# Optimization experiments

Measured on AMD Instinct MI355X. Metric: run time of the kernel, lower is better.

## Reference

```python
import jax, jax.numpy as jnp
import numpy as np

B, N, H, O = 2, 512, 128, 32  # batch, n_particles, hidden_dim, obs_dim


def _linear_init(key, out_d, in_d):
    kw, kb = jax.random.split(key)
    s = 1.0 / np.sqrt(in_d)
    W = jax.random.uniform(kw, (out_d, in_d), minval=-s, maxval=s, dtype=jnp.float32)
    b = jax.random.uniform(kb, (out_d,), minval=-s, maxval=s, dtype=jnp.float32)
    return W, b


def setup_inputs() -> dict:
    key = jax.random.key(0)
    ks = jax.random.split(key, 8)
    z = jax.random.normal(ks[0], (B, N, H), dtype=jnp.float32)
    s_t = jax.random.normal(ks[1], (B, N, O), dtype=jnp.float32)
    W1, b1 = _linear_init(ks[2], H, 2 * H)   # relation_mlp layer 0
    W2, b2 = _linear_init(ks[3], H, H)       # relation_mlp layer 2
    Wq, bq = _linear_init(ks[4], H, H)       # query_proj
    Wk, bk = _linear_init(ks[5], H, O)       # key_proj
    W3, b3 = _linear_init(ks[6], H, H)       # aggregation_mlp layer 0
    W4, b4 = _linear_init(ks[7], H, H)       # aggregation_mlp layer 2
    return dict(z=z, s_t=s_t, W1=W1, b1=b1, W2=W2, b2=b2, Wq=Wq, bq=bq,
                Wk=Wk, bk=bk, W3=W3, b3=b3, W4=W4, b4=b4)


def reference(z, s_t, W1, b1, W2, b2, Wq, bq, Wk, bk, W3, b3, W4, b4):
    b_, n, h = z.shape
    # query depends only on i, key only on j (repeat in the original is redundant)
    q = z @ Wq.T + bq            # [B,N,H]
    k = s_t @ Wk.T + bk          # [B,N,H]
    scores = jnp.einsum('bih,bjh->bij', q, k) / (h ** 0.5)   # [B,N,N]
    eye = jnp.eye(n, dtype=bool)
    scores = jnp.where(eye, -jnp.inf, scores)
    attn = jax.nn.softmax(scores, axis=-1)                   # [B,N,N]
    # relation_mlp on concat(z_i, z_j): split first weight into i- and j- halves
    W1i, W1j = W1[:, :h], W1[:, h:]
    zi = z @ W1i.T               # [B,N,H]
    zj = z @ W1j.T               # [B,N,H]
    rel = jnp.tanh(zi[:, :, None, :] + zj[:, None, :, :] + b1) @ W2.T + b2  # [B,N,N,H]
    agg = jnp.einsum('bij,bijh->bih', attn, rel)             # weighted sum over j
    dz_dt = jnp.tanh(agg @ W3.T + b3) @ W4.T + b4
    return dz_dt
```

## Files before the change

### kernel.cpp

```cpp
#include <hip/hip_runtime.h>
#include <hip/hip_bf16.h>

#define NN 512
#define HH 128
#define OO 32

#define KL 2.8853900817779268f

__device__ __forceinline__ float vexp2(float x) {
    float r; asm("v_exp_f32 %0, %1" : "=v"(r) : "v"(x)); return r;
}
__device__ __forceinline__ float vrcp(float x) {
    float r; asm("v_rcp_f32 %0, %1" : "=v"(r) : "v"(x)); return r;
}
__device__ __forceinline__ float tanh_fast(float x) {
    float e = vexp2(KL * x);
    return 1.0f - 2.0f * vrcp(e + 1.0f);
}
__device__ __forceinline__ float red8(float v) {
    v += __shfl_xor(v, 1, 64); v += __shfl_xor(v, 2, 64); v += __shfl_xor(v, 4, 64);
    return v;
}
__device__ __forceinline__ float dot16r(const float4* w, const float* x, int rot) {
    float a = 0;
#pragma unroll
    for (int ii = 0; ii < 4; ii++) {
        int i = (ii + rot) & 3;
        float4 xv = *(const float4*)(x + i * 4);
        a = fmaf(xv.x, w[ii].x, a); a = fmaf(xv.y, w[ii].y, a);
        a = fmaf(xv.z, w[ii].z, a); a = fmaf(xv.w, w[ii].w, a);
    }
    return a;
}
__device__ __forceinline__ unsigned short f2bf(float x) {
    unsigned u = __float_as_uint(x);
    u += 0x7fffu + ((u >> 16) & 1u);
    return (unsigned short)(u >> 16);
}
__device__ __forceinline__ float bf_lo(unsigned u) { return __uint_as_float((u & 0xffffu) << 16); }
__device__ __forceinline__ float bf_hi(unsigned u) { return __uint_as_float(u & 0xffff0000u); }

__global__ __launch_bounds__(1024, 4) void prep_kernel(
    const float* __restrict__ z, const float* __restrict__ s_t,
    const float* __restrict__ W1, const float* __restrict__ b1,
    const float* __restrict__ Wq, const float* __restrict__ bq,
    const float* __restrict__ Wk, const float* __restrict__ bk,
    float* __restrict__ qP, float* __restrict__ cP,
    unsigned short* __restrict__ EzjG, unsigned* __restrict__ kTp) {
    __shared__ float zrow[4][HH];
    __shared__ float srow[4][OO];
    int t = threadIdx.x, bid = blockIdx.x;
    int r0 = bid * 4, b = bid >> 7, i0 = (bid & 127) * 4;
    int kq = t & 7, h = t >> 3, rot = (kq >> 1) & 3;

    const float4* WqP = (const float4*)(Wq + (size_t)h * HH) + kq * 4;
    const float4* WiP = (const float4*)(W1 + (size_t)h * 2 * HH) + kq * 4;
    const float4* WjP = (const float4*)(W1 + (size_t)h * 2 * HH + HH) + kq * 4;
    float4 wq[4], wi[4], wj[4];
#pragma unroll
    for (int ii = 0; ii < 4; ii++) {
        wq[ii] = WqP[(ii + rot) & 3];
        wi[ii] = WiP[(ii + rot) & 3];
        wj[ii] = WjP[(ii + rot) & 3];
    }
    float4 wk = ((const float4*)(Wk + (size_t)h * OO))[kq];
    float vbq = bq[h], vb1 = b1[h], vbk = bk[h];

    if (t < 4 * HH) zrow[t >> 7][t & 127] = z[(size_t)r0 * HH + t];
    else if (t < 4 * HH + 4 * OO) {
        int u = t - 4 * HH;
        srow[u >> 5][u & 31] = s_t[(size_t)r0 * OO + u];
    }
    __syncthreads();

    {
        float a0 = red8(dot16r(wq, &zrow[0][kq * 16], rot));
        float a1 = red8(dot16r(wq, &zrow[1][kq * 16], rot));
        float a2 = red8(dot16r(wq, &zrow[2][kq * 16], rot));
        float a3 = red8(dot16r(wq, &zrow[3][kq * 16], rot));
        if (kq == 0) {
            float* qp = qP + (size_t)bid * 512 + h * 4;
            qp[0] = a0 + vbq; qp[1] = a1 + vbq; qp[2] = a2 + vbq; qp[3] = a3 + vbq;
        }
    }
    {
        float a0 = red8(dot16r(wi, &zrow[0][kq * 16], rot));
        float a1 = red8(dot16r(wi, &zrow[1][kq * 16], rot));
        float a2 = red8(dot16r(wi, &zrow[2][kq * 16], rot));
        float a3 = red8(dot16r(wi, &zrow[3][kq * 16], rot));
        if (kq == 0) {
            float* cp = cP + (size_t)bid * 512 + h * 4;
            cp[0] = vexp2(KL * (a0 + vb1)); cp[1] = vexp2(KL * (a1 + vb1));
            cp[2] = vexp2(KL * (a2 + vb1)); cp[3] = vexp2(KL * (a3 + vb1));
        }
    }
    {
        float a0 = red8(dot16r(wj, &zrow[0][kq * 16], rot));
        float a1 = red8(dot16r(wj, &zrow[1][kq * 16], rot));
        float a2 = red8(dot16r(wj, &zrow[2][kq * 16], rot));
        float a3 = red8(dot16r(wj, &zrow[3][kq * 16], rot));
        if (kq == 0) {
            EzjG[(size_t)(r0 + 0) * HH + h] = f2bf(vexp2(KL * a0));
            EzjG[(size_t)(r0 + 1) * HH + h] = f2bf(vexp2(KL * a1));
            EzjG[(size_t)(r0 + 2) * HH + h] = f2bf(vexp2(KL * a2));
            EzjG[(size_t)(r0 + 3) * HH + h] = f2bf(vexp2(KL * a3));
        }
    }
    {
        float4 s0 = *(const float4*)&srow[0][kq * 4];
        float4 s1 = *(const float4*)&srow[1][kq * 4];
        float4 s2 = *(const float4*)&srow[2][kq * 4];
        float4 s3 = *(const float4*)&srow[3][kq * 4];
        float a0 = red8(s0.x * wk.x + s0.y * wk.y + s0.z * wk.z + s0.w * wk.w);
        float a1 = red8(s1.x * wk.x + s1.y * wk.y + s1.z * wk.z + s1.w * wk.w);
        float a2 = red8(s2.x * wk.x + s2.y * wk.y + s2.z * wk.z + s2.w * wk.w);
        float a3 = red8(s3.x * wk.x + s3.y * wk.y + s3.z * wk.z + s3.w * wk.w);
        if (kq == 0) {
            unsigned p01 = (unsigned)f2bf(a0 + vbk) | ((unsigned)f2bf(a1 + vbk) << 16);
            unsigned p23 = (unsigned)f2bf(a2 + vbk) | ((unsigned)f2bf(a3 + vbk) << 16);
            unsigned* kp = kTp + ((size_t)b * HH + h) * 256 + (i0 >> 1);
            kp[0] = p01; kp[1] = p23;
        }
    }
}

__global__ __launch_bounds__(1024, 4) void fused_kernel(
    const float* __restrict__ qP, const float* __restrict__ cP,
    const unsigned* __restrict__ kTp, const unsigned short* __restrict__ EzjG,
    const float* __restrict__ W2, const float* __restrict__ b2,
    const float* __restrict__ W3, const float* __restrict__ b3,
    const float* __restrict__ W4, const float* __restrict__ b4,
    float* __restrict__ out) {
    __shared__ float q4T[HH][4];
    __shared__ float c4T[HH][4];
    __shared__ float eBuf[16][4][32];
    __shared__ float sliceS[16][4];
    __shared__ float part[16][4][HH];
    __shared__ float UL[4][HH];
    __shared__ float aggL[4][HH];
    __shared__ float h1L[4][HH];

    int t = threadIdx.x, bid = blockIdx.x;
    int b = bid >> 7, i0 = (bid & 127) * 4, r0 = bid * 4;
    int w = t >> 6, lane = t & 63;

    if (t < 512) ((float*)q4T)[t] = qP[(size_t)bid * 512 + t];
    else         ((float*)c4T)[t - 512] = cP[(size_t)bid * 512 + (t - 512)];
    __syncthreads();

    {
        int jp_local = lane & 15, hq = lane >> 4;
        int jp = w * 16 + jp_local, h0 = hq * 32;
        const unsigned* kb = kTp + ((size_t)b * HH + h0) * 256 + jp;
        float s0l = 0, s1l = 0, s2l = 0, s3l = 0;
        float s0h = 0, s1h = 0, s2h = 0, s3h = 0;
#pragma unroll 8
        for (int hh = 0; hh < 32; hh++) {
            unsigned u = kb[(size_t)hh * 256];
            float kl = bf_lo(u), kh = bf_hi(u);
            float4 qv = *(const float4*)q4T[h0 + hh];
            s0l = fmaf(qv.x, kl, s0l); s1l = fmaf(qv.y, kl, s1l);
            s2l = fmaf(qv.z, kl, s2l); s3l = fmaf(qv.w, kl, s3l);
            s0h = fmaf(qv.x, kh, s0h); s1h = fmaf(qv.y, kh, s1h);
            s2h = fmaf(qv.z, kh, s2h); s3h = fmaf(qv.w, kh, s3h);
        }
        s0l += __shfl_xor(s0l, 16, 64); s0l += __shfl_xor(s0l, 32, 64);
        s1l += __shfl_xor(s1l, 16, 64); s1l += __shfl_xor(s1l, 32, 64);
        s2l += __shfl_xor(s2l, 16, 64); s2l += __shfl_xor(s2l, 32, 64);
        s3l += __shfl_xor(s3l, 16, 64); s3l += __shfl_xor(s3l, 32, 64);
        s0h += __shfl_xor(s0h, 16, 64); s0h += __shfl_xor(s0h, 32, 64);
        s1h += __shfl_xor(s1h, 16, 64); s1h += __shfl_xor(s1h, 32, 64);
        s2h += __shfl_xor(s2h, 16, 64); s2h += __shfl_xor(s2h, 32, 64);
        s3h += __shfl_xor(s3h, 16, 64); s3h += __shfl_xor(s3h, 32, 64);

        const float sc = 0.08838834764831845f;
        float e0l = __expf(s0l * sc), e1l = __expf(s1l * sc);
        float e2l = __expf(s2l * sc), e3l = __expf(s3l * sc);
        float e0h = __expf(s0h * sc), e1h = __expf(s1h * sc);
        float e2h = __expf(s2h * sc), e3h = __expf(s3h * sc);
        int jl = jp * 2, jh = jl + 1;
        if (jl == i0 + 0) e0l = 0.0f;  if (jh == i0 + 0) e0h = 0.0f;
        if (jl == i0 + 1) e1l = 0.0f;  if (jh == i0 + 1) e1h = 0.0f;
        if (jl == i0 + 2) e2l = 0.0f;  if (jh == i0 + 2) e2h = 0.0f;
        if (jl == i0 + 3) e3l = 0.0f;  if (jh == i0 + 3) e3h = 0.0f;

        float ts0 = e0l + e0h, ts1 = e1l + e1h, ts2 = e2l + e2h, ts3 = e3l + e3h;
#pragma unroll
        for (int m = 1; m <= 8; m <<= 1) {
            ts0 += __shfl_xor(ts0, m, 64); ts1 += __shfl_xor(ts1, m, 64);
            ts2 += __shfl_xor(ts2, m, 64); ts3 += __shfl_xor(ts3, m, 64);
        }
        if (lane == 0) {
            sliceS[w][0] = ts0; sliceS[w][1] = ts1;
            sliceS[w][2] = ts2; sliceS[w][3] = ts3;
        }
        if (hq == 0) {
            *(float2*)&eBuf[w][0][2 * jp_local] = make_float2(e0l, e0h);
            *(float2*)&eBuf[w][1][2 * jp_local] = make_float2(e1l, e1h);
            *(float2*)&eBuf[w][2][2 * jp_local] = make_float2(e2l, e2h);
            *(float2*)&eBuf[w][3][2 * jp_local] = make_float2(e3l, e3h);
        }

        int hp = lane * 2, jb = w * 32;
        const unsigned* zbU = (const unsigned*)EzjG + (size_t)b * NN * 64 + lane;
        float4 cA = *(const float4*)c4T[hp];
        float4 cB = *(const float4*)c4T[hp + 1];
        float a0A = 0, a1A = 0, a2A = 0, a3A = 0;
        float a0B = 0, a1B = 0, a2B = 0, a3B = 0;
#pragma unroll 8
        for (int jj = 0; jj < 32; jj++) {
            unsigned u = zbU[(size_t)(jb + jj) * 64];
            float Ex = bf_lo(u), Ey = bf_hi(u);
            float w0 = eBuf[w][0][jj], w1 = eBuf[w][1][jj];
            float w2 = eBuf[w][2][jj], w3 = eBuf[w][3][jj];
            a0A = fmaf(w0, vrcp(fmaf(cA.x, Ex, 1.0f)), a0A);
            a1A = fmaf(w1, vrcp(fmaf(cA.y, Ex, 1.0f)), a1A);
            a2A = fmaf(w2, vrcp(fmaf(cA.z, Ex, 1.0f)), a2A);
            a3A = fmaf(w3, vrcp(fmaf(cA.w, Ex, 1.0f)), a3A);
            a0B = fmaf(w0, vrcp(fmaf(cB.x, Ey, 1.0f)), a0B);
            a1B = fmaf(w1, vrcp(fmaf(cB.y, Ey, 1.0f)), a1B);
            a2B = fmaf(w2, vrcp(fmaf(cB.z, Ey, 1.0f)), a2B);
            a3B = fmaf(w3, vrcp(fmaf(cB.w, Ey, 1.0f)), a3B);
        }
        *(float2*)&part[w][0][hp] = make_float2(a0A, a0B);
        *(float2*)&part[w][1][hp] = make_float2(a1A, a1B);
        *(float2*)&part[w][2][hp] = make_float2(a2A, a2B);
        *(float2*)&part[w][3][hp] = make_float2(a3A, a3B);
    }
    __syncthreads();

    if (t < 512) {
        int r = t >> 7, h = t & 127;
        float s = 0, S = 0;
#pragma unroll
        for (int q = 0; q < 16; q++) { s += part[q][r][h]; S += sliceS[q][r]; }
        UL[r][h] = fmaf(-2.0f * vrcp(S), s, 1.0f);
    }
    __syncthreads();

    {
        int kq = t & 7, h8 = t >> 3, rot = (kq >> 1) & 3;
        float4 wv[4];
        {
            const float4* Wp = (const float4*)(W2 + (size_t)h8 * HH) + kq * 4;
#pragma unroll
            for (int ii = 0; ii < 4; ii++) wv[ii] = Wp[(ii + rot) & 3];
            float a0 = red8(dot16r(wv, &UL[0][kq * 16], rot));
            float a1 = red8(dot16r(wv, &UL[1][kq * 16], rot));
            float a2 = red8(dot16r(wv, &UL[2][kq * 16], rot));
            float a3 = red8(dot16r(wv, &UL[3][kq * 16], rot));
            if (kq == 0) {
                float vb = b2[h8];
                aggL[0][h8] = a0 + vb; aggL[1][h8] = a1 + vb;
                aggL[2][h8] = a2 + vb; aggL[3][h8] = a3 + vb;
            }
        }
        __syncthreads();
        {
            const float4* Wp = (const float4*)(W3 + (size_t)h8 * HH) + kq * 4;
#pragma unroll
            for (int ii = 0; ii < 4; ii++) wv[ii] = Wp[(ii + rot) & 3];
            float a0 = red8(dot16r(wv, &aggL[0][kq * 16], rot));
            float a1 = red8(dot16r(wv, &aggL[1][kq * 16], rot));
            float a2 = red8(dot16r(wv, &aggL[2][kq * 16], rot));
            float a3 = red8(dot16r(wv, &aggL[3][kq * 16], rot));
            if (kq == 0) {
                float vb = b3[h8];
                h1L[0][h8] = tanh_fast(a0 + vb); h1L[1][h8] = tanh_fast(a1 + vb);
                h1L[2][h8] = tanh_fast(a2 + vb); h1L[3][h8] = tanh_fast(a3 + vb);
            }
        }
        __syncthreads();
        {
            const float4* Wp = (const float4*)(W4 + (size_t)h8 * HH) + kq * 4;
#pragma unroll
            for (int ii = 0; ii < 4; ii++) wv[ii] = Wp[(ii + rot) & 3];
            float a0 = red8(dot16r(wv, &h1L[0][kq * 16], rot));
            float a1 = red8(dot16r(wv, &h1L[1][kq * 16], rot));
            float a2 = red8(dot16r(wv, &h1L[2][kq * 16], rot));
            float a3 = red8(dot16r(wv, &h1L[3][kq * 16], rot));
            if (kq == 0) {
                float vb = b4[h8];
                out[(size_t)(r0 + 0) * HH + h8] = a0 + vb;
                out[(size_t)(r0 + 1) * HH + h8] = a1 + vb;
                out[(size_t)(r0 + 2) * HH + h8] = a2 + vb;
                out[(size_t)(r0 + 3) * HH + h8] = a3 + vb;
            }
        }
    }
}

extern "C" void kernel_launch(void* const* d_in, const int* in_sizes, int n_in,
                              void* d_out, int out_size, void* d_ws, size_t ws_size,
                              hipStream_t stream) {
    const float* z   = (const float*)d_in[0];
    const float* s_t = (const float*)d_in[1];
    const float* W1  = (const float*)d_in[2];
    const float* b1  = (const float*)d_in[3];
    const float* W2  = (const float*)d_in[4];
    const float* b2  = (const float*)d_in[5];
    const float* Wq  = (const float*)d_in[6];
    const float* bq  = (const float*)d_in[7];
    const float* Wk  = (const float*)d_in[8];
    const float* bk  = (const float*)d_in[9];
    const float* W3  = (const float*)d_in[10];
    const float* b3  = (const float*)d_in[11];
    const float* W4  = (const float*)d_in[12];
    const float* b4  = (const float*)d_in[13];
    float* out = (float*)d_out;

    float* ws = (float*)d_ws;
    unsigned* kTp = (unsigned*)ws;
    float* qP = ws + 65536;
    float* cP = ws + 196608;
    unsigned short* Ezj = (unsigned short*)(ws + 327680);

    hipLaunchKernelGGL(prep_kernel, dim3(256), dim3(1024), 0, stream,
                       z, s_t, W1, b1, Wq, bq, Wk, bk, qP, cP, Ezj, kTp);
    hipLaunchKernelGGL(fused_kernel, dim3(256), dim3(1024), 0, stream,
                       qP, cP, kTp, Ezj, W2, b2, W3, b3, W4, b4, out);
}
```

Before: 34.52 us.

## Fold key projection into query side and compute scores directly from s_t

Attention scores are rewritten as s_t·(Wkᵀq) plus s_t·(Wkᵀbq). Terms that are constant over j, the bk contributions, are dropped because softmax cancels them. The prep kernel now emits a 32-wide projected query per row instead of 128-wide queries and a transposed bf16 key matrix. The fused kernel therefore does a 32-length dot per (i,j) instead of a 128-length one. The Ezj tile is also prefetched into registers before the first barrier, adding register pressure (32 extra VGPRs) that may affect occupancy.

Measured after the change: 36.40 us. 1.05x slower.

```diff
diff --git a/kernel.cpp b/kernel.cpp
--- a/kernel.cpp
+++ b/kernel.cpp
@@ -6,6 +6,7 @@
 #define OO 32
 
 #define KL 2.8853900817779268f
+#define SCL 0.1275174172f
 
 __device__ __forceinline__ float vexp2(float x) {
     float r; asm("v_exp_f32 %0, %1" : "=v"(r) : "v"(x)); return r;
@@ -16,6 +17,11 @@
 __device__ __forceinline__ float tanh_fast(float x) {
     float e = vexp2(KL * x);
     return 1.0f - 2.0f * vrcp(e + 1.0f);
+}
+__device__ __forceinline__ float waveRedSum(float v) {
+#pragma unroll
+    for (int off = 32; off > 0; off >>= 1) v += __shfl_xor(v, off, 64);
+    return v;
 }
 __device__ __forceinline__ float red8(float v) {
     v += __shfl_xor(v, 1, 64); v += __shfl_xor(v, 2, 64); v += __shfl_xor(v, 4, 64);
@@ -41,16 +47,16 @@
 __device__ __forceinline__ float bf_hi(unsigned u) { return __uint_as_float(u & 0xffff0000u); }
 
 __global__ __launch_bounds__(1024, 4) void prep_kernel(
-    const float* __restrict__ z, const float* __restrict__ s_t,
+    const float* __restrict__ z,
     const float* __restrict__ W1, const float* __restrict__ b1,
-    const float* __restrict__ Wq, const float* __restrict__ bq,
-    const float* __restrict__ Wk, const float* __restrict__ bk,
-    float* __restrict__ qP, float* __restrict__ cP,
-    unsigned short* __restrict__ EzjG, unsigned* __restrict__ kTp) {
+    const float* __restrict__ Wq, const float* __restrict__ Wk,
+    const float* __restrict__ bq,
+    float* __restrict__ cP, unsigned short* __restrict__ EzjG,
+    float* __restrict__ vP, float* __restrict__ gdG) {
     __shared__ float zrow[4][HH];
-    __shared__ float srow[4][OO];
+    __shared__ float qL[4][HH];
     int t = threadIdx.x, bid = blockIdx.x;
-    int r0 = bid * 4, b = bid >> 7, i0 = (bid & 127) * 4;
+    int r0 = bid * 4;
     int kq = t & 7, h = t >> 3, rot = (kq >> 1) & 3;
 
     const float4* WqP = (const float4*)(Wq + (size_t)h * HH) + kq * 4;
@@ -63,14 +69,9 @@
         wi[ii] = WiP[(ii + rot) & 3];
         wj[ii] = WjP[(ii + rot) & 3];
     }
-    float4 wk = ((const float4*)(Wk + (size_t)h * OO))[kq];
-    float vbq = bq[h], vb1 = b1[h], vbk = bk[h];
+    float vb1 = b1[h];
 
     if (t < 4 * HH) zrow[t >> 7][t & 127] = z[(size_t)r0 * HH + t];
-    else if (t < 4 * HH + 4 * OO) {
-        int u = t - 4 * HH;
-        srow[u >> 5][u & 31] = s_t[(size_t)r0 * OO + u];
-    }
     __syncthreads();
 
     {
@@ -78,10 +79,7 @@
         float a1 = red8(dot16r(wq, &zrow[1][kq * 16], rot));
         float a2 = red8(dot16r(wq, &zrow[2][kq * 16], rot));
         float a3 = red8(dot16r(wq, &zrow[3][kq * 16], rot));
-        if (kq == 0) {
-            float* qp = qP + (size_t)bid * 512 + h * 4;
-            qp[0] = a0 + vbq; qp[1] = a1 + vbq; qp[2] = a2 + vbq; qp[3] = a3 + vbq;
-        }
+        if (kq == 0) { qL[0][h] = a0; qL[1][h] = a1; qL[2][h] = a2; qL[3][h] = a3; }
     }
     {
         float a0 = red8(dot16r(wi, &zrow[0][kq * 16], rot));
@@ -106,113 +104,100 @@
             EzjG[(size_t)(r0 + 3) * HH + h] = f2bf(vexp2(KL * a3));
         }
     }
-    {
-        float4 s0 = *(const float4*)&srow[0][kq * 4];
-        float4 s1 = *(const float4*)&srow[1][kq * 4];
-        float4 s2 = *(const float4*)&srow[2][kq * 4];
-        float4 s3 = *(const float4*)&srow[3][kq * 4];
-        float a0 = red8(s0.x * wk.x + s0.y * wk.y + s0.z * wk.z + s0.w * wk.w);
-        float a1 = red8(s1.x * wk.x + s1.y * wk.y + s1.z * wk.z + s1.w * wk.w);
-        float a2 = red8(s2.x * wk.x + s2.y * wk.y + s2.z * wk.z + s2.w * wk.w);
-        float a3 = red8(s3.x * wk.x + s3.y * wk.y + s3.z * wk.z + s3.w * wk.w);
-        if (kq == 0) {
-            unsigned p01 = (unsigned)f2bf(a0 + vbk) | ((unsigned)f2bf(a1 + vbk) << 16);
-            unsigned p23 = (unsigned)f2bf(a2 + vbk) | ((unsigned)f2bf(a3 + vbk) << 16);
-            unsigned* kp = kTp + ((size_t)b * HH + h) * 256 + (i0 >> 1);
-            kp[0] = p01; kp[1] = p23;
-        }
+    __syncthreads();
+
+    if (t < 512) {
+        int r = t >> 7, g = t & 127, o = g >> 2, aq = g & 3;
+        float acc = 0;
+        int a0 = aq * 32;
+#pragma unroll 8
+        for (int a = a0; a < a0 + 32; a++)
+            acc = fmaf(qL[r][a], Wk[(size_t)a * OO + o], acc);
+        acc += __shfl_xor(acc, 1, 64);
+        acc += __shfl_xor(acc, 2, 64);
+        if (aq == 0) vP[(size_t)bid * 128 + o * 4 + r] = acc * SCL;
+    } else if (bid == 0 && t < 544) {
+        int o = t - 512;
+        float acc = 0;
+#pragma unroll 8
+        for (int a = 0; a < HH; a++)
+            acc = fmaf(bq[a], Wk[(size_t)a * OO + o], acc);
+        gdG[o] = acc * SCL;
     }
 }
 
 __global__ __launch_bounds__(1024, 4) void fused_kernel(
-    const float* __restrict__ qP, const float* __restrict__ cP,
-    const unsigned* __restrict__ kTp, const unsigned short* __restrict__ EzjG,
+    const float* __restrict__ s_t,
+    const float* __restrict__ vP, const float* __restrict__ gdG,
+    const float* __restrict__ cP, const unsigned short* __restrict__ EzjG,
     const float* __restrict__ W2, const float* __restrict__ b2,
     const float* __restrict__ W3, const float* __restrict__ b3,
     const float* __restrict__ W4, const float* __restrict__ b4,
     float* __restrict__ out) {
-    __shared__ float q4T[HH][4];
+    __shared__ float v4T[OO][4];
+    __shared__ float gdL[OO];
     __shared__ float c4T[HH][4];
-    __shared__ float eBuf[16][4][32];
-    __shared__ float sliceS[16][4];
+    __shared__ float eBuf[4][NN];
+    __shared__ float sliceS[16][2];
     __shared__ float part[16][4][HH];
     __shared__ float UL[4][HH];
     __shared__ float aggL[4][HH];
     __shared__ float h1L[4][HH];
 
     int t = threadIdx.x, bid = blockIdx.x;
-    int b = bid >> 7, i0 = (bid & 127) * 4, r0 = bid * 4;
+    int b = bid >> 7, i0 = (bid & 127) * 4;
     int w = t >> 6, lane = t & 63;
 
-    if (t < 512) ((float*)q4T)[t] = qP[(size_t)bid * 512 + t];
-    else         ((float*)c4T)[t - 512] = cP[(size_t)bid * 512 + (t - 512)];
-    __syncthreads();
-
-    {
-        int jp_local = lane & 15, hq = lane >> 4;
-        int jp = w * 16 + jp_local, h0 = hq * 32;
-        const unsigned* kb = kTp + ((size_t)b * HH + h0) * 256 + jp;
-        float s0l = 0, s1l = 0, s2l = 0, s3l = 0;
-        float s0h = 0, s1h = 0, s2h = 0, s3h = 0;
-#pragma unroll 8
-        for (int hh = 0; hh < 32; hh++) {
-            unsigned u = kb[(size_t)hh * 256];
-            float kl = bf_lo(u), kh = bf_hi(u);
-            float4 qv = *(const float4*)q4T[h0 + hh];
-            s0l = fmaf(qv.x, kl, s0l); s1l = fmaf(qv.y, kl, s1l);
-            s2l = fmaf(qv.z, kl, s2l); s3l = fmaf(qv.w, kl, s3l);
-            s0h = fmaf(qv.x, kh, s0h); s1h = fmaf(qv.y, kh, s1h);
-            s2h = fmaf(qv.z, kh, s2h); s3h = fmaf(qv.w, kh, s3h);
-        }
-        s0l += __shfl_xor(s0l, 16, 64); s0l += __shfl_xor(s0l, 32, 64);
-        s1l += __shfl_xor(s1l, 16, 64); s1l += __shfl_xor(s1l, 32, 64);
-        s2l += __shfl_xor(s2l, 16, 64); s2l += __shfl_xor(s2l, 32, 64);
-        s3l += __shfl_xor(s3l, 16, 64); s3l += __shfl_xor(s3l, 32, 64);
-        s0h += __shfl_xor(s0h, 16, 64); s0h += __shfl_xor(s0h, 32, 64);
-        s1h += __shfl_xor(s1h, 16, 64); s1h += __shfl_xor(s1h, 32, 64);
-        s2h += __shfl_xor(s2h, 16, 64); s2h += __shfl_xor(s2h, 32, 64);
-        s3h += __shfl_xor(s3h, 16, 64); s3h += __shfl_xor(s3h, 32, 64);
-
-        const float sc = 0.08838834764831845f;
-        float e0l = __expf(s0l * sc), e1l = __expf(s1l * sc);
-        float e2l = __expf(s2l * sc), e3l = __expf(s3l * sc);
-        float e0h = __expf(s0h * sc), e1h = __expf(s1h * sc);
-        float e2h = __expf(s2h * sc), e3h = __expf(s3h * sc);
-        int jl = jp * 2, jh = jl + 1;
-        if (jl == i0 + 0) e0l = 0.0f;  if (jh == i0 + 0) e0h = 0.0f;
-        if (jl == i0 + 1) e1l = 0.0f;  if (jh == i0 + 1) e1h = 0.0f;
-        if (jl == i0 + 2) e2l = 0.0f;  if (jh == i0 + 2) e2h = 0.0f;
-        if (jl == i0 + 3) e3l = 0.0f;  if (jh == i0 + 3) e3h = 0.0f;
-
-        float ts0 = e0l + e0h, ts1 = e1l + e1h, ts2 = e2l + e2h, ts3 = e3l + e3h;
-#pragma unroll
-        for (int m = 1; m <= 8; m <<= 1) {
-            ts0 += __shfl_xor(ts0, m, 64); ts1 += __shfl_xor(ts1, m, 64);
-            ts2 += __shfl_xor(ts2, m, 64); ts3 += __shfl_xor(ts3, m, 64);
-        }
-        if (lane == 0) {
-            sliceS[w][0] = ts0; sliceS[w][1] = ts1;
-            sliceS[w][2] = ts2; sliceS[w][3] = ts3;
-        }
-        if (hq == 0) {
-            *(float2*)&eBuf[w][0][2 * jp_local] = make_float2(e0l, e0h);
-            *(float2*)&eBuf[w][1][2 * jp_local] = make_float2(e1l, e1h);
-            *(float2*)&eBuf[w][2][2 * jp_local] = make_float2(e2l, e2h);
-            *(float2*)&eBuf[w][3][2 * jp_local] = make_float2(e3l, e3h);
-        }
-
+    if (t < 128)       ((float*)v4T)[t] = vP[(size_t)bid * 128 + t];
+    else if (t < 160)  gdL[t - 128] = gdG[t - 128];
+    else if (t >= 512) ((float*)c4T)[t - 512] = cP[(size_t)bid * 512 + (t - 512)];
+
+    unsigned uv[32];
+    {
+        const unsigned* zbU = (const unsigned*)EzjG + (size_t)b * NN * 64 + lane;
+#pragma unroll
+        for (int jj = 0; jj < 32; jj++) uv[jj] = zbU[(size_t)(w * 32 + jj) * 64];
+    }
+    __syncthreads();
+
+    {
+        int j = t & 511, rp = t >> 9, ra = 2 * rp;
+        const float4* sp = (const float4*)(s_t + ((size_t)b * NN + j) * OO);
+        float d0 = 0, d1 = 0, dd = 0;
+#pragma unroll
+        for (int c = 0; c < 8; c++) {
+            float4 sv = sp[c];
+            int o0 = c * 4;
+            float2 v0 = *(const float2*)&v4T[o0 + 0][ra];
+            float2 v1 = *(const float2*)&v4T[o0 + 1][ra];
+            float2 v2 = *(const float2*)&v4T[o0 + 2][ra];
+            float2 v3 = *(const float2*)&v4T[o0 + 3][ra];
+            d0 = fmaf(sv.x, v0.x, d0); d1 = fmaf(sv.x, v0.y, d1); dd = fmaf(sv.x, gdL[o0 + 0], dd);
+            d0 = fmaf(sv.y, v1.x, d0); d1 = fmaf(sv.y, v1.y, d1); dd = fmaf(sv.y, gdL[o0 + 1], dd);
+            d0 = fmaf(sv.z, v2.x, d0); d1 = fmaf(sv.z, v2.y, d1); dd = fmaf(sv.z, gdL[o0 + 2], dd);
+            d0 = fmaf(sv.w, v3.x, d0); d1 = fmaf(sv.w, v3.y, d1); dd = fmaf(sv.w, gdL[o0 + 3], dd);
+        }
+        float e0 = vexp2(d0 + dd), e1 = vexp2(d1 + dd);
+        if (j == i0 + ra)     e0 = 0.0f;
+        if (j == i0 + ra + 1) e1 = 0.0f;
+        eBuf[ra][j] = e0; eBuf[ra + 1][j] = e1;
+        float t0 = waveRedSum(e0), t1 = waveRedSum(e1);
+        if (lane == 0) { sliceS[w][0] = t0; sliceS[w][1] = t1; }
+    }
+    __syncthreads();
+
+    {
         int hp = lane * 2, jb = w * 32;
-        const unsigned* zbU = (const unsigned*)EzjG + (size_t)b * NN * 64 + lane;
         float4 cA = *(const float4*)c4T[hp];
         float4 cB = *(const float4*)c4T[hp + 1];
         float a0A = 0, a1A = 0, a2A = 0, a3A = 0;
         float a0B = 0, a1B = 0, a2B = 0, a3B = 0;
-#pragma unroll 8
+#pragma unroll
         for (int jj = 0; jj < 32; jj++) {
-            unsigned u = zbU[(size_t)(jb + jj) * 64];
-            float Ex = bf_lo(u), Ey = bf_hi(u);
-            float w0 = eBuf[w][0][jj], w1 = eBuf[w][1][jj];
-            float w2 = eBuf[w][2][jj], w3 = eBuf[w][3][jj];
+            int jc = jb + jj;
+            float Ex = bf_lo(uv[jj]), Ey = bf_hi(uv[jj]);
+            float w0 = eBuf[0][jc], w1 = eBuf[1][jc];
+            float w2 = eBuf[2][jc], w3 = eBuf[3][jc];
             a0A = fmaf(w0, vrcp(fmaf(cA.x, Ex, 1.0f)), a0A);
             a1A = fmaf(w1, vrcp(fmaf(cA.y, Ex, 1.0f)), a1A);
             a2A = fmaf(w2, vrcp(fmaf(cA.z, Ex, 1.0f)), a2A);
@@ -231,15 +216,20 @@
 
     if (t < 512) {
         int r = t >> 7, h = t & 127;
-        float s = 0, S = 0;
-#pragma unroll
-        for (int q = 0; q < 16; q++) { s += part[q][r][h]; S += sliceS[q][r]; }
+        float s = 0;
+#pragma unroll
+        for (int q = 0; q < 16; q++) s += part[q][r][h];
+        float S = 0;
+        int wb2 = (r >> 1) * 8, col = r & 1;
+#pragma unroll
+        for (int q = 0; q < 8; q++) S += sliceS[wb2 + q][col];
         UL[r][h] = fmaf(-2.0f * vrcp(S), s, 1.0f);
     }
     __syncthreads();
 
     {
         int kq = t & 7, h8 = t >> 3, rot = (kq >> 1) & 3;
+        int r0 = bid * 4;
         float4 wv[4];
         {
             const float4* Wp = (const float4*)(W2 + (size_t)h8 * HH) + kq * 4;
@@ -308,15 +298,17 @@
     const float* W4  = (const float*)d_in[12];
     const float* b4  = (const float*)d_in[13];
     float* out = (float*)d_out;
+    (void)bk; (void)s_t;
 
     float* ws = (float*)d_ws;
-    unsigned* kTp = (unsigned*)ws;
-    float* qP = ws + 65536;
-    float* cP = ws + 196608;
-    unsigned short* Ezj = (unsigned short*)(ws + 327680);
+    float* cP = ws;
+    float* vP = ws + 131072;
+    float* gdG = ws + 163840;
+    unsigned short* Ezj = (unsigned short*)(ws + 163904);
 
     hipLaunchKernelGGL(prep_kernel, dim3(256), dim3(1024), 0, stream,
-                       z, s_t, W1, b1, Wq, bq, Wk, bk, qP, cP, Ezj, kTp);
+                       z, W1, b1, Wq, Wk, bq, cP, Ezj, vP, gdG);
     hipLaunchKernelGGL(fused_kernel, dim3(256), dim3(1024), 0, stream,
-                       qP, cP, kTp, Ezj, W2, b2, W3, b3, W4, b4, out);
-}
+                       (const float*)d_in[1], vP, gdG, cP, Ezj,
+                       W2, b2, W3, b3, W4, b4, out);
+}
```
